# Kernel tuning notes

Measured on AMD Instinct MI355X. Metric: run time of the kernel, lower is better.

## Reference

```python
import jax, jax.numpy as jnp
import numpy as np

N_NODES = 100000
N_EDGES = 1600000
IN_F, H1, H2, H3, H4, H5, H6, NC = 512, 512, 256, 64, 64, 64, 64, 40


def _linear_params(key, fan_in, fan_out):
    k1, k2 = jax.random.split(key)
    bound = 1.0 / np.sqrt(fan_in)
    W = jax.random.uniform(k1, (fan_in, fan_out), minval=-bound, maxval=bound, dtype=jnp.float32)
    b = jax.random.uniform(k2, (fan_out,), minval=-bound, maxval=bound, dtype=jnp.float32)
    return W, b


def setup_inputs() -> dict:
    key = jax.random.key(0)
    ks = jax.random.split(key, 10)
    x = jax.random.normal(ks[0], (N_NODES, IN_F), dtype=jnp.float32)
    src = jax.random.randint(ks[1], (N_EDGES,), 0, N_NODES, dtype=jnp.int32)
    dst = jax.random.randint(ks[2], (N_EDGES,), 0, N_NODES, dtype=jnp.int32)
    W1, b1 = _linear_params(ks[3], IN_F, H1)
    W2, b2 = _linear_params(ks[4], H1, H2)
    W3, b3 = _linear_params(ks[5], H2, H3)
    Wg1, bg1 = _linear_params(ks[6], H3, H4)
    Wg2, bg2 = _linear_params(ks[7], H4, H5)
    Wg3, bg3 = _linear_params(ks[8], H5, H6)
    Wg4, bg4 = _linear_params(ks[9], H6, NC)
    return {"x": x, "src": src, "dst": dst,
            "W1": W1, "b1": b1, "W2": W2, "b2": b2, "W3": W3, "b3": b3,
            "Wg1": Wg1, "bg1": bg1, "Wg2": Wg2, "bg2": bg2,
            "Wg3": Wg3, "bg3": bg3, "Wg4": Wg4, "bg4": bg4}


def _graph_conv(h, src, dst, norm_src, norm_dst, W, b):
    # DGL GraphConv, norm='both': D_dst^{-1/2} A D_src^{-1/2} H W + b
    msg = (h * norm_src[:, None])[src]            # [E, d] gather from source nodes
    agg = jax.ops.segment_sum(msg, dst, num_segments=N_NODES)  # scatter-add to dst
    agg = agg * norm_dst[:, None]
    return agg @ W + b


def reference(x, src, dst, W1, b1, W2, b2, W3, b3,
              Wg1, bg1, Wg2, bg2, Wg3, bg3, Wg4, bg4):
    ones = jnp.ones((N_EDGES,), dtype=jnp.float32)
    deg_out = jax.ops.segment_sum(ones, src, num_segments=N_NODES)
    deg_in = jax.ops.segment_sum(ones, dst, num_segments=N_NODES)
    norm_src = jax.lax.rsqrt(jnp.clip(deg_out, 1.0))
    norm_dst = jax.lax.rsqrt(jnp.clip(deg_in, 1.0))

    h = jax.nn.relu(x @ W1 + b1)
    h = jax.nn.relu(h @ W2 + b2)
    h = jax.nn.relu(h @ W3 + b3)
    h = jax.nn.relu(_graph_conv(h, src, dst, norm_src, norm_dst, Wg1, bg1))
    h = jax.nn.relu(_graph_conv(h, src, dst, norm_src, norm_dst, Wg2, bg2))
    h = jax.nn.relu(_graph_conv(h, src, dst, norm_src, norm_dst, Wg3, bg3))
    h = jax.nn.relu(_graph_conv(h, src, dst, norm_src, norm_dst, Wg4, bg4))
    return h
```

## Files before the change

### kernel.cpp

```cpp
#include <hip/hip_runtime.h>

#define N_NODES 100000
#define N_EDGES 1600000
#define M_PAD   100096
#define BCAP    64
#define X_REAL 51200000L
#define X_PAD  ((long)M_PAD*512)

typedef __bf16 bf16x8 __attribute__((ext_vector_type(8)));
typedef float  f32x4  __attribute__((ext_vector_type(4)));
typedef unsigned short u16x8 __attribute__((ext_vector_type(8)));

__device__ __forceinline__ unsigned short f2bf(float f) {
  union { float f; unsigned u; } x; x.f = f;
  unsigned r = (x.u + 0x7FFFu + ((x.u >> 16) & 1u)) >> 16;
  return (unsigned short)r;
}

__device__ __forceinline__ float bf2f(unsigned short h) {
  union { unsigned u; float f; } x; x.u = ((unsigned)h) << 16;
  return x.f;
}

__device__ __forceinline__ void async_copy16(const void* g, void* l) {
  __builtin_amdgcn_global_load_lds((__attribute__((address_space(1))) void*)g,
                                   (__attribute__((address_space(3))) void*)l,
                                   16, 0, 0);
}


__global__ void cvt_x_kernel(const float* __restrict__ x, unsigned short* __restrict__ xb) {
  long e = ((long)blockIdx.x * 256 + threadIdx.x) * 8;
  u16x8 o;
  if (e < X_REAL) {
    float4 f0 = *(const float4*)(x + e);
    float4 f1 = *(const float4*)(x + e + 4);
    o[0] = f2bf(f0.x); o[1] = f2bf(f0.y); o[2] = f2bf(f0.z); o[3] = f2bf(f0.w);
    o[4] = f2bf(f1.x); o[5] = f2bf(f1.y); o[6] = f2bf(f1.z); o[7] = f2bf(f1.w);
  } else {
    o = (u16x8)0;
  }
  *(u16x8*)(xb + e) = o;
}

__global__ void cvt_wt_kernel(const float* __restrict__ W, unsigned short* __restrict__ Wt,
                              int K, int N, int Npad) {
  int idx = blockIdx.x * 256 + threadIdx.x;
  if (idx >= Npad * K) return;
  int n = idx / K, k = idx % K;
  Wt[idx] = (n < N) ? f2bf(W[(long)k * N + n]) : (unsigned short)0;
}

__global__ void cvt_wt_dup_kernel(const float* __restrict__ W, unsigned short* __restrict__ Wt,
                                  int N) {
  int idx = blockIdx.x * 256 + threadIdx.x;
  if (idx >= 64 * 128) return;
  int n = idx >> 7, k = idx & 127;
  Wt[idx] = (n < N) ? f2bf(W[(long)(k & 63) * N + n]) : (unsigned short)0;
}

__global__ void norms_kernel(const int* __restrict__ hist,
                             float* __restrict__ nsrc, float* __restrict__ ndst) {
  int i = blockIdx.x * 256 + threadIdx.x;
  if (i >= M_PAD) return;
  if (i < N_NODES) {
    nsrc[i] = rsqrtf(fmaxf((float)hist[N_NODES + i], 1.f));
    ndst[i] = rsqrtf(fmaxf((float)hist[i], 1.f));
  } else {
    nsrc[i] = 1.f;
  }
}

template <int BM, int BN, int BK, int EPI, bool EDGES, int TPB>
__launch_bounds__(TPB)
__global__ void gemm_bt(const unsigned short* __restrict__ A,
                        const unsigned short* __restrict__ Bt,
                        const float* __restrict__ bias,
                        const float* __restrict__ rowscale,
                        void* __restrict__ C, int K, int Nfull,
                        const int* __restrict__ esrc, const int* __restrict__ edst,
                        int* __restrict__ hist, int* __restrict__ bucket) {
  if constexpr (EDGES) {
    if (blockIdx.x == gridDim.x - 1) {
      const int S = gridDim.y * TPB;
      int e = blockIdx.y * TPB + threadIdx.x;
      for (; e + 3 * S < N_EDGES; e += 4 * S) {
        int s0 = esrc[e],         d0 = edst[e];
        int s1 = esrc[e + S],     d1 = edst[e + S];
        int s2 = esrc[e + 2 * S], d2 = edst[e + 2 * S];
        int s3 = esrc[e + 3 * S], d3 = edst[e + 3 * S];
        atomicAdd(&hist[N_NODES + s0], 1);
        atomicAdd(&hist[N_NODES + s1], 1);
        atomicAdd(&hist[N_NODES + s2], 1);
        atomicAdd(&hist[N_NODES + s3], 1);
        int p0 = atomicAdd(&hist[d0], 1);
        int p1 = atomicAdd(&hist[d1], 1);
        int p2 = atomicAdd(&hist[d2], 1);
        int p3 = atomicAdd(&hist[d3], 1);
        if (p0 < BCAP) bucket[(size_t)d0 * BCAP + p0] = s0;
        if (p1 < BCAP) bucket[(size_t)d1 * BCAP + p1] = s1;
        if (p2 < BCAP) bucket[(size_t)d2 * BCAP + p2] = s2;
        if (p3 < BCAP) bucket[(size_t)d3 * BCAP + p3] = s3;
      }
      for (; e < N_EDGES; e += S) {
        int s = esrc[e], d = edst[e];
        atomicAdd(&hist[N_NODES + s], 1);
        int p = atomicAdd(&hist[d], 1);
        if (p < BCAP) bucket[(size_t)d * BCAP + p] = s;
      }
      return;
    }
  }
  constexpr int WAVES = TPB / 64;
  constexpr int WAVES_M = 2, WAVES_N = WAVES / 2;
  constexpr int WM = BM / WAVES_M, WN = BN / WAVES_N;
  constexpr int MI = WM / 16, NI = WN / 16;
  __shared__ __align__(16) unsigned short As[BM * BK];
  __shared__ __align__(16) unsigned short Bs[BN * BK];
  const int tid = threadIdx.x;
  const int wave = tid >> 6, lane = tid & 63;
  const int wm0 = (wave / WAVES_N) * WM, wn0 = (wave % WAVES_N) * WN;
  const long rowBase = (long)blockIdx.y * BM;
  const int colBase = blockIdx.x * BN;
  const unsigned short* Ab = A + rowBase * K;
  const unsigned short* Bb = Bt + (long)colBase * K;
  f32x4 acc[MI][NI] = {};
  constexpr int ACH = BM * BK / 8;
  constexpr int BCH = BN * BK / 8;
  for (int k0 = 0; k0 < K; k0 += BK) {
#pragma unroll
    for (int c = tid; c < ACH; c += TPB) {
      int r = (c * 8) / BK, cc = (c * 8) % BK;
      async_copy16(Ab + (long)r * K + k0 + cc, &As[c * 8]);
    }
#pragma unroll
    for (int c = tid; c < BCH; c += TPB) {
      int r = (c * 8) / BK, cc = (c * 8) % BK;
      async_copy16(Bb + (long)r * K + k0 + cc, &Bs[c * 8]);
    }
    __syncthreads();
#pragma unroll
    for (int kk = 0; kk < BK; kk += 32) {
      bf16x8 af[MI], bfr[NI];
#pragma unroll
      for (int mi = 0; mi < MI; ++mi)
        af[mi] = *(const bf16x8*)&As[(wm0 + mi * 16 + (lane & 15)) * BK + kk + (lane >> 4) * 8];
#pragma unroll
      for (int ni = 0; ni < NI; ++ni)
        bfr[ni] = *(const bf16x8*)&Bs[(wn0 + ni * 16 + (lane & 15)) * BK + kk + (lane >> 4) * 8];
#pragma unroll
      for (int mi = 0; mi < MI; ++mi)
#pragma unroll
        for (int ni = 0; ni < NI; ++ni)
          acc[mi][ni] = __builtin_amdgcn_mfma_f32_16x16x32_bf16(af[mi], bfr[ni], acc[mi][ni], 0, 0, 0);
    }
    __syncthreads();
  }
  const int q = lane >> 4, c15 = lane & 15;
#pragma unroll
  for (int mi = 0; mi < MI; ++mi) {
#pragma unroll
    for (int ni = 0; ni < NI; ++ni) {
#pragma unroll
      for (int r = 0; r < 4; ++r) {
        long row = rowBase + wm0 + mi * 16 + q * 4 + r;
        int col = colBase + wn0 + ni * 16 + c15;
        float v = acc[mi][ni][r];
        if constexpr (EPI == 0) {
          v = fmaxf(v + bias[col], 0.f);
          ((unsigned short*)C)[row * Nfull + col] = f2bf(v);
        } else if constexpr (EPI == 1) {
          v = fmaxf(v + bias[col], 0.f) * rowscale[row];
          ((unsigned short*)C)[row * Nfull + col] = f2bf(v);
        } else {
          float bv = (col < 40) ? bias[col] : 0.f;
          float vv = fmaxf(v + bv, 0.f);
          if (row < N_NODES && col < 40)
            ((float*)C)[row * 40 + col] = vv;
        }
      }
    }
  }
}

__global__ void agg_kernel(const unsigned short* __restrict__ u,
                           const int* __restrict__ bucket, const int* __restrict__ cnt,
                           const float* __restrict__ ndst,
                           unsigned short* __restrict__ za) {
  const int node = blockIdx.x * 4 + (threadIdx.x >> 6);
  const int lane = threadIdx.x & 63;
  const int r8 = lane >> 3;
  const int c8 = (lane & 7) * 8;
  float a0 = 0.f, a1 = 0.f, a2 = 0.f, a3 = 0.f, a4 = 0.f, a5 = 0.f, a6 = 0.f, a7 = 0.f;
  int n = 0;
  if (node < N_NODES) n = min(cnt[node], BCAP);
  const int* bk = bucket + (size_t)node * BCAP;
#pragma unroll 2
  for (int i = r8; i < n; i += 8) {
    int s = bk[i];
    u16x8 v = *(const u16x8*)(u + (size_t)s * 64 + c8);
    a0 += bf2f(v[0]); a1 += bf2f(v[1]); a2 += bf2f(v[2]); a3 += bf2f(v[3]);
    a4 += bf2f(v[4]); a5 += bf2f(v[5]); a6 += bf2f(v[6]); a7 += bf2f(v[7]);
  }
#pragma unroll
  for (int m = 8; m <= 32; m <<= 1) {
    a0 += __shfl_xor(a0, m); a1 += __shfl_xor(a1, m);
    a2 += __shfl_xor(a2, m); a3 += __shfl_xor(a3, m);
    a4 += __shfl_xor(a4, m); a5 += __shfl_xor(a5, m);
    a6 += __shfl_xor(a6, m); a7 += __shfl_xor(a7, m);
  }
  if (r8 == 0) {
    float nd = (node < N_NODES) ? ndst[node] : 0.f;
    float vv[8] = {nd * a0, nd * a1, nd * a2, nd * a3, nd * a4, nd * a5, nd * a6, nd * a7};
    u16x8 H, L;
#pragma unroll
    for (int t = 0; t < 8; ++t) {
      unsigned short h = f2bf(vv[t]);
      H[t] = h;
      L[t] = f2bf(vv[t] - bf2f(h));
    }
    *(u16x8*)(za + (size_t)node * 128 + c8) = H;
    *(u16x8*)(za + (size_t)node * 128 + 64 + c8) = L;
  }
}


extern "C" void kernel_launch(void* const* d_in, const int* in_sizes, int n_in,
                              void* d_out, int out_size, void* d_ws, size_t ws_size,
                              hipStream_t stream) {
  (void)in_sizes; (void)n_in; (void)out_size; (void)ws_size;
  const float* x   = (const float*)d_in[0];
  const int* esrc  = (const int*)d_in[1];
  const int* edst  = (const int*)d_in[2];
  const float* W1  = (const float*)d_in[3];  const float* b1  = (const float*)d_in[4];
  const float* W2  = (const float*)d_in[5];  const float* b2  = (const float*)d_in[6];
  const float* W3  = (const float*)d_in[7];  const float* b3  = (const float*)d_in[8];
  const float* Wg1 = (const float*)d_in[9];  const float* bg1 = (const float*)d_in[10];
  const float* Wg2 = (const float*)d_in[11]; const float* bg2 = (const float*)d_in[12];
  const float* Wg3 = (const float*)d_in[13]; const float* bg3 = (const float*)d_in[14];
  const float* Wg4 = (const float*)d_in[15]; const float* bg4 = (const float*)d_in[16];
  float* out = (float*)d_out;

  char* ws = (char*)d_ws;
  size_t off = 0;
  auto alloc = [&](size_t bytes) -> void* {
    void* p = ws + off;
    off += (bytes + 255) & ~(size_t)255;
    return p;
  };

  unsigned short* xb = (unsigned short*)alloc((size_t)M_PAD * 512 * 2);
  unsigned short* h1 = (unsigned short*)alloc((size_t)M_PAD * 512 * 2);
  int*   bucket  = (int*)alloc((size_t)N_NODES * BCAP * 4);
  int*   hist    = (int*)alloc((size_t)2 * N_NODES * 4);
  float* nsrc    = (float*)alloc((size_t)M_PAD * 4);
  float* ndst    = (float*)alloc((size_t)N_NODES * 4);
  unsigned short* W1t  = (unsigned short*)alloc(512 * 512 * 2);
  unsigned short* W2t  = (unsigned short*)alloc(256 * 512 * 2);
  unsigned short* W3t  = (unsigned short*)alloc(64 * 256 * 2);
  unsigned short* Wg1t = (unsigned short*)alloc(64 * 128 * 2);
  unsigned short* Wg2t = (unsigned short*)alloc(64 * 128 * 2);
  unsigned short* Wg3t = (unsigned short*)alloc(64 * 128 * 2);
  unsigned short* Wg4t = (unsigned short*)alloc(64 * 128 * 2);

  unsigned short* h2 = xb;
  unsigned short* U0 = (unsigned short*)((char*)xb + (size_t)M_PAD * 256 * 2);
  unsigned short* U1 = (unsigned short*)((char*)U0 + (size_t)M_PAD * 64 * 2);
  unsigned short* za = (unsigned short*)((char*)U1 + (size_t)M_PAD * 64 * 2);

  hipMemsetAsync(hist, 0, (size_t)2 * N_NODES * 4, stream);

  cvt_x_kernel<<<(int)(X_PAD / 8 / 256), 256, 0, stream>>>(x, xb);

  cvt_wt_kernel<<<(512 * 512 + 255) / 256, 256, 0, stream>>>(W1, W1t, 512, 512, 512);
  cvt_wt_kernel<<<(256 * 512 + 255) / 256, 256, 0, stream>>>(W2, W2t, 512, 256, 256);
  cvt_wt_kernel<<<(64 * 256 + 255) / 256, 256, 0, stream>>>(W3, W3t, 256, 64, 64);
  cvt_wt_dup_kernel<<<(64 * 128 + 255) / 256, 256, 0, stream>>>(Wg1, Wg1t, 64);
  cvt_wt_dup_kernel<<<(64 * 128 + 255) / 256, 256, 0, stream>>>(Wg2, Wg2t, 64);
  cvt_wt_dup_kernel<<<(64 * 128 + 255) / 256, 256, 0, stream>>>(Wg3, Wg3t, 64);
  cvt_wt_dup_kernel<<<(64 * 128 + 255) / 256, 256, 0, stream>>>(Wg4, Wg4t, 40);

  const int GY = M_PAD / 128;

  gemm_bt<128, 256, 64, 0, true, 512><<<dim3(3, GY), 512, 0, stream>>>(
      xb, W1t, b1, nullptr, h1, 512, 512, esrc, edst, hist, bucket);

  norms_kernel<<<(M_PAD + 255) / 256, 256, 0, stream>>>(hist, nsrc, ndst);

  gemm_bt<128, 256, 64, 0, false, 512><<<dim3(1, GY), 512, 0, stream>>>(
      h1, W2t, b2, nullptr, h2, 512, 256, nullptr, nullptr, nullptr, nullptr);
  gemm_bt<128, 64, 64, 1, false, 256><<<dim3(1, GY), 256, 0, stream>>>(
      h2, W3t, b3, nsrc, U0, 256, 64, nullptr, nullptr, nullptr, nullptr);

  agg_kernel<<<M_PAD / 4, 256, 0, stream>>>(U0, bucket, hist, ndst, za);
  gemm_bt<128, 64, 64, 1, false, 256><<<dim3(1, GY), 256, 0, stream>>>(
      za, Wg1t, bg1, nsrc, U1, 128, 64, nullptr, nullptr, nullptr, nullptr);

  agg_kernel<<<M_PAD / 4, 256, 0, stream>>>(U1, bucket, hist, ndst, za);
  gemm_bt<128, 64, 64, 1, false, 256><<<dim3(1, GY), 256, 0, stream>>>(
      za, Wg2t, bg2, nsrc, U0, 128, 64, nullptr, nullptr, nullptr, nullptr);

  agg_kernel<<<M_PAD / 4, 256, 0, stream>>>(U0, bucket, hist, ndst, za);
  gemm_bt<128, 64, 64, 1, false, 256><<<dim3(1, GY), 256, 0, stream>>>(
      za, Wg3t, bg3, nsrc, U1, 128, 64, nullptr, nullptr, nullptr, nullptr);

  agg_kernel<<<M_PAD / 4, 256, 0, stream>>>(U1, bucket, hist, ndst, za);
  gemm_bt<128, 64, 64, 4, false, 256><<<dim3(1, GY), 256, 0, stream>>>(
      za, Wg4t, bg4, nullptr, out, 128, 64, nullptr, nullptr, nullptr, nullptr);
}
```

Measured before the change: 788.7 us.

## Fuse three MLP GEMMs into one kernel keeping intermediates in LDS

Replaces the three separate MLP GEMM launches with one kernel. Each 64-row block computes layer 1, keeps the 512-wide activation in swizzled LDS, then runs layers 2 and 3 from LDS and writes only the 64-wide output. Edge bucketing moves into a second grid column of this kernel. Because norms are not ready yet, the source-norm scaling moves into the first aggregation via a per-edge nsrc lookup. This removes the h1/h2 global round trips, but every block reloads the full W1 and W2 weights, and the large LDS footprint (~104KB) limits occupancy.

```diff
diff --git a/kernel.cpp b/kernel.cpp
--- a/kernel.cpp
+++ b/kernel.cpp
@@ -4,6 +4,7 @@
 #define N_EDGES 1600000
 #define M_PAD   100096
 #define BCAP    64
+#define EBLK    782
 #define X_REAL 51200000L
 #define X_PAD  ((long)M_PAD*512)
 
@@ -26,6 +27,13 @@
   __builtin_amdgcn_global_load_lds((__attribute__((address_space(1))) void*)g,
                                    (__attribute__((address_space(3))) void*)l,
                                    16, 0, 0);
+}
+
+__device__ __forceinline__ int swz1(int row, int col) {
+  return ((row * 1024 + col * 2) ^ ((row & 7) << 4)) >> 1;
+}
+__device__ __forceinline__ int swz2(int row, int col) {
+  return ((row * 512 + col * 2) ^ ((row & 7) << 4)) >> 1;
 }
 
 
@@ -71,46 +79,174 @@
   }
 }
 
-template <int BM, int BN, int BK, int EPI, bool EDGES, int TPB>
+__launch_bounds__(512)
+__global__ void fused_mlp(const unsigned short* __restrict__ xb,
+                          const unsigned short* __restrict__ W1t,
+                          const unsigned short* __restrict__ W2t,
+                          const unsigned short* __restrict__ W3t,
+                          const float* __restrict__ b1,
+                          const float* __restrict__ b2,
+                          const float* __restrict__ b3,
+                          unsigned short* __restrict__ u0,
+                          const int* __restrict__ esrc, const int* __restrict__ edst,
+                          int* __restrict__ hist, int* __restrict__ bucket) {
+  if (blockIdx.x == 1) {
+    if (blockIdx.y >= EBLK) return;
+    const int S = EBLK * 512;
+    int e = blockIdx.y * 512 + (int)threadIdx.x;
+    for (; e + 3 * S < N_EDGES; e += 4 * S) {
+      int s0 = esrc[e],         d0 = edst[e];
+      int s1 = esrc[e + S],     d1 = edst[e + S];
+      int s2 = esrc[e + 2 * S], d2 = edst[e + 2 * S];
+      int s3 = esrc[e + 3 * S], d3 = edst[e + 3 * S];
+      atomicAdd(&hist[N_NODES + s0], 1);
+      atomicAdd(&hist[N_NODES + s1], 1);
+      atomicAdd(&hist[N_NODES + s2], 1);
+      atomicAdd(&hist[N_NODES + s3], 1);
+      int p0 = atomicAdd(&hist[d0], 1);
+      int p1 = atomicAdd(&hist[d1], 1);
+      int p2 = atomicAdd(&hist[d2], 1);
+      int p3 = atomicAdd(&hist[d3], 1);
+      if (p0 < BCAP) bucket[(size_t)d0 * BCAP + p0] = s0;
+      if (p1 < BCAP) bucket[(size_t)d1 * BCAP + p1] = s1;
+      if (p2 < BCAP) bucket[(size_t)d2 * BCAP + p2] = s2;
+      if (p3 < BCAP) bucket[(size_t)d3 * BCAP + p3] = s3;
+    }
+    for (; e < N_EDGES; e += S) {
+      int s = esrc[e], d = edst[e];
+      atomicAdd(&hist[N_NODES + s], 1);
+      int p = atomicAdd(&hist[d], 1);
+      if (p < BCAP) bucket[(size_t)d * BCAP + p] = s;
+    }
+    return;
+  }
+  __shared__ __align__(16) unsigned short Xs[64 * 64];
+  __shared__ __align__(16) unsigned short Wb[64 * 512];
+  __shared__ __align__(16) unsigned short W2s[256 * 64];
+  const int tid = threadIdx.x;
+  const int wave = tid >> 6, lane = tid & 63;
+  const int l15 = lane & 15, l4 = lane >> 4;
+  const int wm0 = (wave >> 2) * 32;
+  const int wnA = (wave & 3) * 128, wnB = (wave & 3) * 64, wnC = (wave & 3) * 16;
+  const long rowBase = (long)blockIdx.y * 64;
+
+  float b1c[8], b2c[4];
+#pragma unroll
+  for (int ni = 0; ni < 8; ++ni) b1c[ni] = b1[wnA + ni * 16 + l15];
+#pragma unroll
+  for (int ni = 0; ni < 4; ++ni) b2c[ni] = b2[wnB + ni * 16 + l15];
+  const float b3c = b3[wnC + l15];
+
+  f32x4 acc1[2][8] = {};
+  for (int k0 = 0; k0 < 512; k0 += 64) {
+    {
+      int r = tid >> 3, cc = (tid & 7) * 8;
+      async_copy16(xb + (rowBase + r) * 512 + k0 + cc, &Xs[tid * 8]);
+    }
+#pragma unroll
+    for (int c = tid; c < 4096; c += 512) {
+      int r = c >> 3, cc = (c & 7) * 8;
+      async_copy16(W1t + (long)r * 512 + k0 + cc, &Wb[c * 8]);
+    }
+    __syncthreads();
+#pragma unroll
+    for (int kk = 0; kk < 64; kk += 32) {
+      bf16x8 af[2], bfr[8];
+#pragma unroll
+      for (int mi = 0; mi < 2; ++mi)
+        af[mi] = *(const bf16x8*)&Xs[(wm0 + mi * 16 + l15) * 64 + kk + l4 * 8];
+#pragma unroll
+      for (int ni = 0; ni < 8; ++ni)
+        bfr[ni] = *(const bf16x8*)&Wb[(wnA + ni * 16 + l15) * 64 + kk + l4 * 8];
+#pragma unroll
+      for (int mi = 0; mi < 2; ++mi)
+#pragma unroll
+        for (int ni = 0; ni < 8; ++ni)
+          acc1[mi][ni] = __builtin_amdgcn_mfma_f32_16x16x32_bf16(af[mi], bfr[ni], acc1[mi][ni], 0, 0, 0);
+    }
+    __syncthreads();
+  }
+#pragma unroll
+  for (int mi = 0; mi < 2; ++mi)
+#pragma unroll
+    for (int ni = 0; ni < 8; ++ni)
+#pragma unroll
+      for (int r = 0; r < 4; ++r) {
+        int row = wm0 + mi * 16 + l4 * 4 + r;
+        int col = wnA + ni * 16 + l15;
+        Wb[swz1(row, col)] = f2bf(fmaxf(acc1[mi][ni][r] + b1c[ni], 0.f));
+      }
+  __syncthreads();
+
+  f32x4 acc2[2][4] = {};
+  for (int k0 = 0; k0 < 512; k0 += 64) {
+#pragma unroll
+    for (int c = tid; c < 2048; c += 512) {
+      int r = c >> 3, cc = (c & 7) * 8;
+      async_copy16(W2t + (long)r * 512 + k0 + cc, &W2s[c * 8]);
+    }
+    __syncthreads();
+#pragma unroll
+    for (int kk = 0; kk < 64; kk += 32) {
+      bf16x8 af[2], bfr[4];
+#pragma unroll
+      for (int mi = 0; mi < 2; ++mi)
+        af[mi] = *(const bf16x8*)&Wb[swz1(wm0 + mi * 16 + l15, k0 + kk + l4 * 8)];
+#pragma unroll
+      for (int ni = 0; ni < 4; ++ni)
+        bfr[ni] = *(const bf16x8*)&W2s[(wnB + ni * 16 + l15) * 64 + kk + l4 * 8];
+#pragma unroll
+      for (int mi = 0; mi < 2; ++mi)
+#pragma unroll
+        for (int ni = 0; ni < 4; ++ni)
+          acc2[mi][ni] = __builtin_amdgcn_mfma_f32_16x16x32_bf16(af[mi], bfr[ni], acc2[mi][ni], 0, 0, 0);
+    }
+    __syncthreads();
+  }
+#pragma unroll
+  for (int mi = 0; mi < 2; ++mi)
+#pragma unroll
+    for (int ni = 0; ni < 4; ++ni)
+#pragma unroll
+      for (int r = 0; r < 4; ++r) {
+        int row = wm0 + mi * 16 + l4 * 4 + r;
+        int col = wnB + ni * 16 + l15;
+        Wb[swz2(row, col)] = f2bf(fmaxf(acc2[mi][ni][r] + b2c[ni], 0.f));
+      }
+  __syncthreads();
+
+#pragma unroll
+  for (int c = tid; c < 2048; c += 512)
+    async_copy16(W3t + c * 8, &W2s[c * 8]);
+  __syncthreads();
+  f32x4 acc3[2] = {};
+#pragma unroll
+  for (int kk = 0; kk < 256; kk += 32) {
+    bf16x8 af[2], bfr;
+    bfr = *(const bf16x8*)&W2s[(wnC + l15) * 256 + kk + l4 * 8];
+#pragma unroll
+    for (int mi = 0; mi < 2; ++mi) {
+      af[mi] = *(const bf16x8*)&Wb[swz2(wm0 + mi * 16 + l15, kk + l4 * 8)];
+      acc3[mi] = __builtin_amdgcn_mfma_f32_16x16x32_bf16(af[mi], bfr, acc3[mi], 0, 0, 0);
+    }
+  }
+#pragma unroll
+  for (int mi = 0; mi < 2; ++mi)
+#pragma unroll
+    for (int r = 0; r < 4; ++r) {
+      long row = rowBase + wm0 + mi * 16 + l4 * 4 + r;
+      int col = wnC + l15;
+      u0[row * 64 + col] = f2bf(fmaxf(acc3[mi][r] + b3c, 0.f));
+    }
+}
+
+template <int BM, int BN, int BK, int EPI, int TPB>
 __launch_bounds__(TPB)
 __global__ void gemm_bt(const unsigned short* __restrict__ A,
                         const unsigned short* __restrict__ Bt,
                         const float* __restrict__ bias,
                         const float* __restrict__ rowscale,
-                        void* __restrict__ C, int K, int Nfull,
-                        const int* __restrict__ esrc, const int* __restrict__ edst,
-                        int* __restrict__ hist, int* __restrict__ bucket) {
-  if constexpr (EDGES) {
-    if (blockIdx.x == gridDim.x - 1) {
-      const int S = gridDim.y * TPB;
-      int e = blockIdx.y * TPB + threadIdx.x;
-      for (; e + 3 * S < N_EDGES; e += 4 * S) {
-        int s0 = esrc[e],         d0 = edst[e];
-        int s1 = esrc[e + S],     d1 = edst[e + S];
-        int s2 = esrc[e + 2 * S], d2 = edst[e + 2 * S];
-        int s3 = esrc[e + 3 * S], d3 = edst[e + 3 * S];
-        atomicAdd(&hist[N_NODES + s0], 1);
-        atomicAdd(&hist[N_NODES + s1], 1);
-        atomicAdd(&hist[N_NODES + s2], 1);
-        atomicAdd(&hist[N_NODES + s3], 1);
-        int p0 = atomicAdd(&hist[d0], 1);
-        int p1 = atomicAdd(&hist[d1], 1);
-        int p2 = atomicAdd(&hist[d2], 1);
-        int p3 = atomicAdd(&hist[d3], 1);
-        if (p0 < BCAP) bucket[(size_t)d0 * BCAP + p0] = s0;
-        if (p1 < BCAP) bucket[(size_t)d1 * BCAP + p1] = s1;
-        if (p2 < BCAP) bucket[(size_t)d2 * BCAP + p2] = s2;
-        if (p3 < BCAP) bucket[(size_t)d3 * BCAP + p3] = s3;
-      }
-      for (; e < N_EDGES; e += S) {
-        int s = esrc[e], d = edst[e];
-        atomicAdd(&hist[N_NODES + s], 1);
-        int p = atomicAdd(&hist[d], 1);
-        if (p < BCAP) bucket[(size_t)d * BCAP + p] = s;
-      }
-      return;
-    }
-  }
+                        void* __restrict__ C, int K, int Nfull) {
   constexpr int WAVES = TPB / 64;
   constexpr int WAVES_M = 2, WAVES_N = WAVES / 2;
   constexpr int WM = BM / WAVES_M, WN = BN / WAVES_N;
@@ -166,10 +302,7 @@
         long row = rowBase + wm0 + mi * 16 + q * 4 + r;
         int col = colBase + wn0 + ni * 16 + c15;
         float v = acc[mi][ni][r];
-        if constexpr (EPI == 0) {
-          v = fmaxf(v + bias[col], 0.f);
-          ((unsigned short*)C)[row * Nfull + col] = f2bf(v);
-        } else if constexpr (EPI == 1) {
+        if constexpr (EPI == 1) {
           v = fmaxf(v + bias[col], 0.f) * rowscale[row];
           ((unsigned short*)C)[row * Nfull + col] = f2bf(v);
         } else {
@@ -183,10 +316,13 @@
   }
 }
 
-__global__ void agg_kernel(const unsigned short* __restrict__ u,
-                           const int* __restrict__ bucket, const int* __restrict__ cnt,
-                           const float* __restrict__ ndst,
-                           unsigned short* __restrict__ za) {
+__device__ __forceinline__ void agg_body(const unsigned short* __restrict__ u,
+                                         const int* __restrict__ bucket,
+                                         const int* __restrict__ cnt,
+                                         const float* __restrict__ ndst,
+                                         const float* __restrict__ nsrc,
+                                         unsigned short* __restrict__ za,
+                                         const int SCALE_SRC) {
   const int node = blockIdx.x * 4 + (threadIdx.x >> 6);
   const int lane = threadIdx.x & 63;
   const int r8 = lane >> 3;
@@ -198,9 +334,10 @@
 #pragma unroll 2
   for (int i = r8; i < n; i += 8) {
     int s = bk[i];
+    float w = SCALE_SRC ? nsrc[s] : 1.f;
     u16x8 v = *(const u16x8*)(u + (size_t)s * 64 + c8);
-    a0 += bf2f(v[0]); a1 += bf2f(v[1]); a2 += bf2f(v[2]); a3 += bf2f(v[3]);
-    a4 += bf2f(v[4]); a5 += bf2f(v[5]); a6 += bf2f(v[6]); a7 += bf2f(v[7]);
+    a0 += w * bf2f(v[0]); a1 += w * bf2f(v[1]); a2 += w * bf2f(v[2]); a3 += w * bf2f(v[3]);
+    a4 += w * bf2f(v[4]); a5 += w * bf2f(v[5]); a6 += w * bf2f(v[6]); a7 += w * bf2f(v[7]);
   }
 #pragma unroll
   for (int m = 8; m <= 32; m <<= 1) {
@@ -222,6 +359,14 @@
     *(u16x8*)(za + (size_t)node * 128 + c8) = H;
     *(u16x8*)(za + (size_t)node * 128 + 64 + c8) = L;
   }
+}
+
+template <int SCALE_SRC>
+__global__ void agg_kernel(const unsigned short* __restrict__ u,
+                           const int* __restrict__ bucket, const int* __restrict__ cnt,
+                           const float* __restrict__ ndst, const float* __restrict__ nsrc,
+                           unsigned short* __restrict__ za) {
+  agg_body(u, bucket, cnt, ndst, nsrc, za, SCALE_SRC);
 }
 
 
@@ -250,7 +395,7 @@
   };
 
   unsigned short* xb = (unsigned short*)alloc((size_t)M_PAD * 512 * 2);
-  unsigned short* h1 = (unsigned short*)alloc((size_t)M_PAD * 512 * 2);
+  unsigned short* r1 = (unsigned short*)alloc((size_t)M_PAD * 512 * 2);
   int*   bucket  = (int*)alloc((size_t)N_NODES * BCAP * 4);
   int*   hist    = (int*)alloc((size_t)2 * N_NODES * 4);
   float* nsrc    = (float*)alloc((size_t)M_PAD * 4);
@@ -263,10 +408,9 @@
   unsigned short* Wg3t = (unsigned short*)alloc(64 * 128 * 2);
   unsigned short* Wg4t = (unsigned short*)alloc(64 * 128 * 2);
 
-  unsigned short* h2 = xb;
-  unsigned short* U0 = (unsigned short*)((char*)xb + (size_t)M_PAD * 256 * 2);
-  unsigned short* U1 = (unsigned short*)((char*)U0 + (size_t)M_PAD * 64 * 2);
-  unsigned short* za = (unsigned short*)((char*)U1 + (size_t)M_PAD * 64 * 2);
+  unsigned short* U0 = r1;
+  unsigned short* U1 = r1 + (size_t)M_PAD * 64;
+  unsigned short* za = r1 + (size_t)M_PAD * 128;
 
   hipMemsetAsync(hist, 0, (size_t)2 * N_NODES * 4, stream);
 
@@ -280,31 +424,26 @@
   cvt_wt_dup_kernel<<<(64 * 128 + 255) / 256, 256, 0, stream>>>(Wg3, Wg3t, 64);
   cvt_wt_dup_kernel<<<(64 * 128 + 255) / 256, 256, 0, stream>>>(Wg4, Wg4t, 40);
 
+  fused_mlp<<<dim3(2, M_PAD / 64), 512, 0, stream>>>(
+      xb, W1t, W2t, W3t, b1, b2, b3, U0, esrc, edst, hist, bucket);
+
+  norms_kernel<<<(M_PAD + 255) / 256, 256, 0, stream>>>(hist, nsrc, ndst);
+
   const int GY = M_PAD / 128;
 
-  gemm_bt<128, 256, 64, 0, true, 512><<<dim3(3, GY), 512, 0, stream>>>(
-      xb, W1t, b1, nullptr, h1, 512, 512, esrc, edst, hist, bucket);
-
-  norms_kernel<<<(M_PAD + 255) / 256, 256, 0, stream>>>(hist, nsrc, ndst);
-
-  gemm_bt<128, 256, 64, 0, false, 512><<<dim3(1, GY), 512, 0, stream>>>(
-      h1, W2t, b2, nullptr, h2, 512, 256, nullptr, nullptr, nullptr, nullptr);
-  gemm_bt<128, 64, 64, 1, false, 256><<<dim3(1, GY), 256, 0, stream>>>(
-      h2, W3t, b3, nsrc, U0, 256, 64, nullptr, nullptr, nullptr, nullptr);
-
-  agg_kernel<<<M_PAD / 4, 256, 0, stream>>>(U0, bucket, hist, ndst, za);
-  gemm_bt<128, 64, 64, 1, false, 256><<<dim3(1, GY), 256, 0, stream>>>(
-      za, Wg1t, bg1, nsrc, U1, 128, 64, nullptr, nullptr, nullptr, nullptr);
-
-  agg_kernel<<<M_PAD / 4, 256, 0, stream>>>(U1, bucket, hist, ndst, za);
-  gemm_bt<128, 64, 64, 1, false, 256><<<dim3(1, GY), 256, 0, stream>>>(
-      za, Wg2t, bg2, nsrc, U0, 128, 64, nullptr, nullptr, nullptr, nullptr);
-
-  agg_kernel<<<M_PAD / 4, 256, 0, stream>>>(U0, bucket, hist, ndst, za);
-  gemm_bt<128, 64, 64, 1, false, 256><<<dim3(1, GY), 256, 0, stream>>>(
-      za, Wg3t, bg3, nsrc, U1, 128, 64, nullptr, nullptr, nullptr, nullptr);
-
-  agg_kernel<<<M_PAD / 4, 256, 0, stream>>>(U1, bucket, hist, ndst, za);
-  gemm_bt<128, 64, 64, 4, false, 256><<<dim3(1, GY), 256, 0, stream>>>(
-      za, Wg4t, bg4, nullptr, out, 128, 64, nullptr, nullptr, nullptr, nullptr);
-}
+  agg_kernel<1><<<M_PAD / 4, 256, 0, stream>>>(U0, bucket, hist, ndst, nsrc, za);
+  gemm_bt<128, 64, 64, 1, 256><<<dim3(1, GY), 256, 0, stream>>>(
+      za, Wg1t, bg1, nsrc, U1, 128, 64);
+
+  agg_kernel<0><<<M_PAD / 4, 256, 0, stream>>>(U1, bucket, hist, ndst, nsrc, za);
+  gemm_bt<128, 64, 64, 1, 256><<<dim3(1, GY), 256, 0, stream>>>(
+      za, Wg2t, bg2, nsrc, U0, 128, 64);
+
+  agg_kernel<0><<<M_PAD / 4, 256, 0, stream>>>(U0, bucket, hist, ndst, nsrc, za);
+  gemm_bt<128, 64, 64, 1, 256><<<dim3(1, GY), 256, 0, stream>>>(
+      za, Wg3t, bg3, nsrc, U1, 128, 64);
+
+  agg_kernel<0><<<M_PAD / 4, 256, 0, stream>>>(U1, bucket, hist, ndst, nsrc, za);
+  gemm_bt<128, 64, 64, 4, 256><<<dim3(1, GY), 256, 0, stream>>>(
+      za, Wg4t, bg4, nullptr, out, 128, 64);
+}
```

Result: slower. 976.5 us (+23.8%).

## Partition edge histogram/bucketing blocks by node range to localize atomics

Applied to the files above, without the earlier changes.

The edge-degree histogram and bucket fill, run by the last column of GEMM blocks, now splits those blocks into 8 groups. Each group owns one eighth of the node range and scans all edges, applying only the atomics whose node falls in its range. The goal is to keep each group's atomics in a narrower address range, likely for better L2/XCD locality with less cross-die contention. In exchange every group reads the full edge arrays, which is 8x the edge loads, and the 4-way unrolling is dropped.

```diff
diff --git a/kernel.cpp b/kernel.cpp
--- a/kernel.cpp
+++ b/kernel.cpp
@@ -82,31 +82,19 @@
                         int* __restrict__ hist, int* __restrict__ bucket) {
   if constexpr (EDGES) {
     if (blockIdx.x == gridDim.x - 1) {
-      const int S = gridDim.y * TPB;
-      int e = blockIdx.y * TPB + threadIdx.x;
-      for (; e + 3 * S < N_EDGES; e += 4 * S) {
-        int s0 = esrc[e],         d0 = edst[e];
-        int s1 = esrc[e + S],     d1 = edst[e + S];
-        int s2 = esrc[e + 2 * S], d2 = edst[e + 2 * S];
-        int s3 = esrc[e + 3 * S], d3 = edst[e + 3 * S];
-        atomicAdd(&hist[N_NODES + s0], 1);
-        atomicAdd(&hist[N_NODES + s1], 1);
-        atomicAdd(&hist[N_NODES + s2], 1);
-        atomicAdd(&hist[N_NODES + s3], 1);
-        int p0 = atomicAdd(&hist[d0], 1);
-        int p1 = atomicAdd(&hist[d1], 1);
-        int p2 = atomicAdd(&hist[d2], 1);
-        int p3 = atomicAdd(&hist[d3], 1);
-        if (p0 < BCAP) bucket[(size_t)d0 * BCAP + p0] = s0;
-        if (p1 < BCAP) bucket[(size_t)d1 * BCAP + p1] = s1;
-        if (p2 < BCAP) bucket[(size_t)d2 * BCAP + p2] = s2;
-        if (p3 < BCAP) bucket[(size_t)d3 * BCAP + p3] = s3;
-      }
-      for (; e < N_EDGES; e += S) {
+      const int grp = blockIdx.y & 7;
+      const int member = blockIdx.y >> 3;
+      const int members = (int)((gridDim.y - grp + 7) >> 3);
+      const int lo = grp * (N_NODES / 8);
+      const int hi = (grp == 7) ? N_NODES : lo + (N_NODES / 8);
+      const int S = members * TPB;
+      for (int e = member * TPB + (int)threadIdx.x; e < N_EDGES; e += S) {
         int s = esrc[e], d = edst[e];
-        atomicAdd(&hist[N_NODES + s], 1);
-        int p = atomicAdd(&hist[d], 1);
-        if (p < BCAP) bucket[(size_t)d * BCAP + p] = s;
+        if (s >= lo && s < hi) atomicAdd(&hist[N_NODES + s], 1);
+        if (d >= lo && d < hi) {
+          int p = atomicAdd(&hist[d], 1);
+          if (p < BCAP) bucket[(size_t)d * BCAP + p] = s;
+        }
       }
       return;
     }
```

Result: slower. 840.3 us (+6.5%).

## Merge x/weight conversion and edge bucketing into one prep kernel

Applied to the files above, without the earlier changes.

Folds the x-to-bf16 conversion, all seven weight transpose/convert launches and the edge histogram/bucket build into a single prep kernel, with block ranges assigned to each task. The edge work that was piggybacked on the first GEMM (as an extra grid column) moves into this prep kernel, so the first GEMM launches only its real tiles. This removes several small launches and lets the atomics-heavy edge pass overlap with the bandwidth-bound x conversion. In exchange, the edge pass no longer overlaps with GEMM compute, and the prep kernel mixes very different workloads in one grid.

```diff
diff --git a/kernel.cpp b/kernel.cpp
--- a/kernel.cpp
+++ b/kernel.cpp
@@ -7,6 +7,13 @@
 #define X_REAL 51200000L
 #define X_PAD  ((long)M_PAD*512)
 
+#define EB     782
+#define XB     12512
+#define WB     864
+#define XOFF   (EB)
+#define WOFF   (EB + XB)
+#define PREP_GRID (EB + XB + WB)
+
 typedef __bf16 bf16x8 __attribute__((ext_vector_type(8)));
 typedef float  f32x4  __attribute__((ext_vector_type(4)));
 typedef unsigned short u16x8 __attribute__((ext_vector_type(8)));
@@ -28,35 +35,81 @@
                                    16, 0, 0);
 }
 
-
-__global__ void cvt_x_kernel(const float* __restrict__ x, unsigned short* __restrict__ xb) {
-  long e = ((long)blockIdx.x * 256 + threadIdx.x) * 8;
-  u16x8 o;
-  if (e < X_REAL) {
-    float4 f0 = *(const float4*)(x + e);
-    float4 f1 = *(const float4*)(x + e + 4);
-    o[0] = f2bf(f0.x); o[1] = f2bf(f0.y); o[2] = f2bf(f0.z); o[3] = f2bf(f0.w);
-    o[4] = f2bf(f1.x); o[5] = f2bf(f1.y); o[6] = f2bf(f1.z); o[7] = f2bf(f1.w);
+__launch_bounds__(512)
+__global__ void prep_kernel(const float* __restrict__ x, unsigned short* __restrict__ xb,
+                            const int* __restrict__ esrc, const int* __restrict__ edst,
+                            int* __restrict__ hist, int* __restrict__ bucket,
+                            const float* __restrict__ W1, unsigned short* __restrict__ W1t,
+                            const float* __restrict__ W2, unsigned short* __restrict__ W2t,
+                            const float* __restrict__ W3, unsigned short* __restrict__ W3t,
+                            const float* __restrict__ Wg1, unsigned short* __restrict__ Wg1t,
+                            const float* __restrict__ Wg2, unsigned short* __restrict__ Wg2t,
+                            const float* __restrict__ Wg3, unsigned short* __restrict__ Wg3t,
+                            const float* __restrict__ Wg4, unsigned short* __restrict__ Wg4t) {
+  const int bx = blockIdx.x;
+  const int tid = threadIdx.x;
+  if (bx < EB) {
+    const int S = EB * 512;
+    int e = bx * 512 + tid;
+    for (; e + 3 * S < N_EDGES; e += 4 * S) {
+      int s0 = esrc[e],         d0 = edst[e];
+      int s1 = esrc[e + S],     d1 = edst[e + S];
+      int s2 = esrc[e + 2 * S], d2 = edst[e + 2 * S];
+      int s3 = esrc[e + 3 * S], d3 = edst[e + 3 * S];
+      atomicAdd(&hist[N_NODES + s0], 1);
+      atomicAdd(&hist[N_NODES + s1], 1);
+      atomicAdd(&hist[N_NODES + s2], 1);
+      atomicAdd(&hist[N_NODES + s3], 1);
+      int p0 = atomicAdd(&hist[d0], 1);
+      int p1 = atomicAdd(&hist[d1], 1);
+      int p2 = atomicAdd(&hist[d2], 1);
+      int p3 = atomicAdd(&hist[d3], 1);
+      if (p0 < BCAP) bucket[(size_t)d0 * BCAP + p0] = s0;
+      if (p1 < BCAP) bucket[(size_t)d1 * BCAP + p1] = s1;
+      if (p2 < BCAP) bucket[(size_t)d2 * BCAP + p2] = s2;
+      if (p3 < BCAP) bucket[(size_t)d3 * BCAP + p3] = s3;
+    }
+    for (; e < N_EDGES; e += S) {
+      int s = esrc[e], d = edst[e];
+      atomicAdd(&hist[N_NODES + s], 1);
+      int p = atomicAdd(&hist[d], 1);
+      if (p < BCAP) bucket[(size_t)d * BCAP + p] = s;
+    }
+    return;
+  }
+  if (bx < WOFF) {
+    long e = ((long)(bx - XOFF) * 512 + tid) * 8;
+    u16x8 o;
+    if (e < X_REAL) {
+      float4 f0 = *(const float4*)(x + e);
+      float4 f1 = *(const float4*)(x + e + 4);
+      o[0] = f2bf(f0.x); o[1] = f2bf(f0.y); o[2] = f2bf(f0.z); o[3] = f2bf(f0.w);
+      o[4] = f2bf(f1.x); o[5] = f2bf(f1.y); o[6] = f2bf(f1.z); o[7] = f2bf(f1.w);
+    } else {
+      o = (u16x8)0;
+    }
+    *(u16x8*)(xb + e) = o;
+    return;
+  }
+  long t = (long)(bx - WOFF) * 512 + tid;
+  if (t < 262144) {
+    int n = (int)(t >> 9), k = (int)(t & 511);
+    W1t[t] = f2bf(W1[(long)k * 512 + n]);
+  } else if ((t -= 262144) < 131072) {
+    int n = (int)(t >> 9), k = (int)(t & 511);
+    W2t[t] = f2bf(W2[(long)k * 256 + n]);
+  } else if ((t -= 131072) < 16384) {
+    int n = (int)(t >> 8), k = (int)(t & 255);
+    W3t[t] = f2bf(W3[(long)k * 64 + n]);
   } else {
-    o = (u16x8)0;
-  }
-  *(u16x8*)(xb + e) = o;
-}
-
-__global__ void cvt_wt_kernel(const float* __restrict__ W, unsigned short* __restrict__ Wt,
-                              int K, int N, int Npad) {
-  int idx = blockIdx.x * 256 + threadIdx.x;
-  if (idx >= Npad * K) return;
-  int n = idx / K, k = idx % K;
-  Wt[idx] = (n < N) ? f2bf(W[(long)k * N + n]) : (unsigned short)0;
-}
-
-__global__ void cvt_wt_dup_kernel(const float* __restrict__ W, unsigned short* __restrict__ Wt,
-                                  int N) {
-  int idx = blockIdx.x * 256 + threadIdx.x;
-  if (idx >= 64 * 128) return;
-  int n = idx >> 7, k = idx & 127;
-  Wt[idx] = (n < N) ? f2bf(W[(long)(k & 63) * N + n]) : (unsigned short)0;
+    t -= 16384;
+    int which = (int)(t >> 13), q = (int)(t & 8191);
+    int n = q >> 7, k = q & 127;
+    const float* src = (which == 0) ? Wg1 : (which == 1) ? Wg2 : (which == 2) ? Wg3 : Wg4;
+    unsigned short* dst = (which == 0) ? Wg1t : (which == 1) ? Wg2t : (which == 2) ? Wg3t : Wg4t;
+    int N = (which == 3) ? 40 : 64;
+    dst[q] = (n < N) ? f2bf(src[(long)(k & 63) * N + n]) : (unsigned short)0;
+  }
 }
 
 __global__ void norms_kernel(const int* __restrict__ hist,
@@ -71,46 +124,13 @@
   }
 }
 
-template <int BM, int BN, int BK, int EPI, bool EDGES, int TPB>
+template <int BM, int BN, int BK, int EPI, int TPB>
 __launch_bounds__(TPB)
 __global__ void gemm_bt(const unsigned short* __restrict__ A,
                         const unsigned short* __restrict__ Bt,
                         const float* __restrict__ bias,
                         const float* __restrict__ rowscale,
-                        void* __restrict__ C, int K, int Nfull,
-                        const int* __restrict__ esrc, const int* __restrict__ edst,
-                        int* __restrict__ hist, int* __restrict__ bucket) {
-  if constexpr (EDGES) {
-    if (blockIdx.x == gridDim.x - 1) {
-      const int S = gridDim.y * TPB;
-      int e = blockIdx.y * TPB + threadIdx.x;
-      for (; e + 3 * S < N_EDGES; e += 4 * S) {
-        int s0 = esrc[e],         d0 = edst[e];
-        int s1 = esrc[e + S],     d1 = edst[e + S];
-        int s2 = esrc[e + 2 * S], d2 = edst[e + 2 * S];
-        int s3 = esrc[e + 3 * S], d3 = edst[e + 3 * S];
-        atomicAdd(&hist[N_NODES + s0], 1);
-        atomicAdd(&hist[N_NODES + s1], 1);
-        atomicAdd(&hist[N_NODES + s2], 1);
-        atomicAdd(&hist[N_NODES + s3], 1);
-        int p0 = atomicAdd(&hist[d0], 1);
-        int p1 = atomicAdd(&hist[d1], 1);
-        int p2 = atomicAdd(&hist[d2], 1);
-        int p3 = atomicAdd(&hist[d3], 1);
-        if (p0 < BCAP) bucket[(size_t)d0 * BCAP + p0] = s0;
-        if (p1 < BCAP) bucket[(size_t)d1 * BCAP + p1] = s1;
-        if (p2 < BCAP) bucket[(size_t)d2 * BCAP + p2] = s2;
-        if (p3 < BCAP) bucket[(size_t)d3 * BCAP + p3] = s3;
-      }
-      for (; e < N_EDGES; e += S) {
-        int s = esrc[e], d = edst[e];
-        atomicAdd(&hist[N_NODES + s], 1);
-        int p = atomicAdd(&hist[d], 1);
-        if (p < BCAP) bucket[(size_t)d * BCAP + p] = s;
-      }
-      return;
-    }
-  }
+                        void* __restrict__ C, int K, int Nfull) {
   constexpr int WAVES = TPB / 64;
   constexpr int WAVES_M = 2, WAVES_N = WAVES / 2;
   constexpr int WM = BM / WAVES_M, WN = BN / WAVES_N;
@@ -270,41 +290,34 @@
 
   hipMemsetAsync(hist, 0, (size_t)2 * N_NODES * 4, stream);
 
-  cvt_x_kernel<<<(int)(X_PAD / 8 / 256), 256, 0, stream>>>(x, xb);
-
-  cvt_wt_kernel<<<(512 * 512 + 255) / 256, 256, 0, stream>>>(W1, W1t, 512, 512, 512);
-  cvt_wt_kernel<<<(256 * 512 + 255) / 256, 256, 0, stream>>>(W2, W2t, 512, 256, 256);
-  cvt_wt_kernel<<<(64 * 256 + 255) / 256, 256, 0, stream>>>(W3, W3t, 256, 64, 64);
-  cvt_wt_dup_kernel<<<(64 * 128 + 255) / 256, 256, 0, stream>>>(Wg1, Wg1t, 64);
-  cvt_wt_dup_kernel<<<(64 * 128 + 255) / 256, 256, 0, stream>>>(Wg2, Wg2t, 64);
-  cvt_wt_dup_kernel<<<(64 * 128 + 255) / 256, 256, 0, stream>>>(Wg3, Wg3t, 64);
-  cvt_wt_dup_kernel<<<(64 * 128 + 255) / 256, 256, 0, stream>>>(Wg4, Wg4t, 40);
+  prep_kernel<<<PREP_GRID, 512, 0, stream>>>(
+      x, xb, esrc, edst, hist, bucket,
+      W1, W1t, W2, W2t, W3, W3t, Wg1, Wg1t, Wg2, Wg2t, Wg3, Wg3t, Wg4, Wg4t);
+
+  norms_kernel<<<(M_PAD + 255) / 256, 256, 0, stream>>>(hist, nsrc, ndst);
 
   const int GY = M_PAD / 128;
 
-  gemm_bt<128, 256, 64, 0, true, 512><<<dim3(3, GY), 512, 0, stream>>>(
-      xb, W1t, b1, nullptr, h1, 512, 512, esrc, edst, hist, bucket);
-
-  norms_kernel<<<(M_PAD + 255) / 256, 256, 0, stream>>>(hist, nsrc, ndst);
-
-  gemm_bt<128, 256, 64, 0, false, 512><<<dim3(1, GY), 512, 0, stream>>>(
-      h1, W2t, b2, nullptr, h2, 512, 256, nullptr, nullptr, nullptr, nullptr);
-  gemm_bt<128, 64, 64, 1, false, 256><<<dim3(1, GY), 256, 0, stream>>>(
-      h2, W3t, b3, nsrc, U0, 256, 64, nullptr, nullptr, nullptr, nullptr);
+  gemm_bt<128, 256, 64, 0, 512><<<dim3(2, GY), 512, 0, stream>>>(
+      xb, W1t, b1, nullptr, h1, 512, 512);
+  gemm_bt<128, 256, 64, 0, 512><<<dim3(1, GY), 512, 0, stream>>>(
+      h1, W2t, b2, nullptr, h2, 512, 256);
+  gemm_bt<128, 64, 64, 1, 256><<<dim3(1, GY), 256, 0, stream>>>(
+      h2, W3t, b3, nsrc, U0, 256, 64);
 
   agg_kernel<<<M_PAD / 4, 256, 0, stream>>>(U0, bucket, hist, ndst, za);
-  gemm_bt<128, 64, 64, 1, false, 256><<<dim3(1, GY), 256, 0, stream>>>(
-      za, Wg1t, bg1, nsrc, U1, 128, 64, nullptr, nullptr, nullptr, nullptr);
+  gemm_bt<128, 64, 64, 1, 256><<<dim3(1, GY), 256, 0, stream>>>(
+      za, Wg1t, bg1, nsrc, U1, 128, 64);
 
   agg_kernel<<<M_PAD / 4, 256, 0, stream>>>(U1, bucket, hist, ndst, za);
-  gemm_bt<128, 64, 64, 1, false, 256><<<dim3(1, GY), 256, 0, stream>>>(
-      za, Wg2t, bg2, nsrc, U0, 128, 64, nullptr, nullptr, nullptr, nullptr);
+  gemm_bt<128, 64, 64, 1, 256><<<dim3(1, GY), 256, 0, stream>>>(
+      za, Wg2t, bg2, nsrc, U0, 128, 64);
 
   agg_kernel<<<M_PAD / 4, 256, 0, stream>>>(U0, bucket, hist, ndst, za);
-  gemm_bt<128, 64, 64, 1, false, 256><<<dim3(1, GY), 256, 0, stream>>>(
-      za, Wg3t, bg3, nsrc, U1, 128, 64, nullptr, nullptr, nullptr, nullptr);
+  gemm_bt<128, 64, 64, 1, 256><<<dim3(1, GY), 256, 0, stream>>>(
+      za, Wg3t, bg3, nsrc, U1, 128, 64);
 
   agg_kernel<<<M_PAD / 4, 256, 0, stream>>>(U1, bucket, hist, ndst, za);
-  gemm_bt<128, 64, 64, 4, false, 256><<<dim3(1, GY), 256, 0, stream>>>(
-      za, Wg4t, bg4, nullptr, out, 128, 64, nullptr, nullptr, nullptr, nullptr);
-}
+  gemm_bt<128, 64, 64, 4, 256><<<dim3(1, GY), 256, 0, stream>>>(
+      za, Wg4t, bg4, nullptr, out, 128, 64);
+}
```

After: 868.4 us. 1.1x slower.
